# Kernel tuning notes

Hardware: AMD Instinct MI355X
Metric: run time of the kernel (lower is better)

## Reference

```python
import jax, jax.numpy as jnp
import numpy as np

PI = float(np.pi)


def _mat(rows):
    # rows: 4 lists of 4 [..., ] arrays -> [..., 4, 4]
    return jnp.stack([jnp.stack(r, axis=-1) for r in rows], axis=-2)


def _local_frames(q):
    """q: [..., 7] joint angles -> list of 8 local [..., 4, 4] transforms."""
    z = jnp.zeros_like(q[..., 0])
    o = jnp.ones_like(z)

    def cs(a):
        return jnp.cos(a), jnp.sin(a)

    c0, s0 = cs(q[..., 0])
    c1, s1 = cs(q[..., 1])
    c2, s2 = cs(q[..., 2] - 0.5 * PI)
    c3, s3 = cs(q[..., 3])
    c4, s4 = cs(q[..., 4])
    c5, s5 = cs(q[..., 5] + 0.5 * PI)
    c6, s6 = cs(q[..., 6] - 0.5 * PI)

    m0 = _mat([[c0, -s0, z, z], [s0, c0, z, z], [z, z, o, z], [z, z, z, o]])
    m1 = _mat([[c1, -s1, z, z], [z, z, -o, z], [s1, c1, z, z], [z, z, z, o]])
    m2 = _mat([[c2, -s2, z, z], [z, z, o, 0.4 * o], [-s2, -c2, z, z], [z, z, z, o]])
    m3 = _mat([[c3, -s3, z, z], [z, z, -o, z], [s3, c3, z, z], [z, z, z, o]])
    m4 = _mat([[-c4, s4, z, z], [z, z, o, 0.39 * o], [s4, c4, z, z], [z, z, z, o]])
    m5 = _mat([[c5, -s5, z, z], [z, z, -o, z], [s5, c5, z, z], [z, z, z, o]])
    m6 = _mat([[c6, -s6, z, z], [z, z, -o, z], [s6, c6, z, z], [z, z, z, o]])
    m7 = _mat([[-o, z, z, z], [z, z, o, 0.118 * o], [z, o, z, z], [z, z, z, o]])
    return [m0, m1, m2, m3, m4, m5, m6, m7]


def setup_inputs() -> dict:
    key = jax.random.key(0)
    x = jax.random.normal(key, (2000000, 7), dtype=jnp.float32)
    return {"x": x}


def reference(x):
    mats = _local_frames(x)
    frames = [mats[0]]
    f = mats[0]
    for m in mats[1:]:  # fixed chain of 7 tiny 4x4 matmuls over batch
        f = jnp.einsum("...ij,...jk->...ik", f, m)
        frames.append(f)
    return jnp.stack(frames, axis=-3)  # [..., 8, 4, 4]
```

## Files before the change

kernel.cpp:

```cpp
#include <hip/hip_runtime.h>

namespace {

struct V3 { float x, y, z; };

__device__ inline V3 v3(float x, float y, float z) { return {x, y, z}; }
__device__ inline V3 vadd(V3 a, V3 b) { return {a.x + b.x, a.y + b.y, a.z + b.z}; }
__device__ inline V3 vsub(V3 a, V3 b) { return {a.x - b.x, a.y - b.y, a.z - b.z}; }
__device__ inline V3 vmul(float s, V3 a) { return {s * a.x, s * a.y, s * a.z}; }
__device__ inline V3 vneg(V3 a) { return {-a.x, -a.y, -a.z}; }

__device__ inline void stage_frame(float4* p, V3 c0, V3 c1, V3 c2, V3 c3) {
    p[0] = make_float4(c0.x, c1.x, c2.x, c3.x);
    p[1] = make_float4(c0.y, c1.y, c2.y, c3.y);
    p[2] = make_float4(c0.z, c1.z, c2.z, c3.z);
    p[3] = make_float4(0.f, 0.f, 0.f, 1.f);
}

}

#define LSTRIDE 33

__global__ __launch_bounds__(64) void fk_chain_kernel(const float* __restrict__ q,
                                                      float4* __restrict__ out,
                                                      int n)
{
    __shared__ float4 lds[64 * LSTRIDE];

    const int lane = threadIdx.x;
    const long long e0 = (long long)blockIdx.x * 64;
    const long long i = e0 + lane;
    const bool active = i < (long long)n;

    const float* qi = q + (active ? i : (long long)(n - 1)) * 7;
    const float HPI = 1.57079632679489662f;

    float qv[7];
    #pragma unroll
    for (int k = 0; k < 7; ++k) qv[k] = qi[k];

    float c[7], s[7];
    __sincosf(qv[0], &s[0], &c[0]);
    __sincosf(qv[1], &s[1], &c[1]);
    __sincosf(qv[2] - HPI, &s[2], &c[2]);
    __sincosf(qv[3], &s[3], &c[3]);
    __sincosf(qv[4], &s[4], &c[4]);
    __sincosf(qv[5] + HPI, &s[5], &c[5]);
    __sincosf(qv[6] - HPI, &s[6], &c[6]);

    float4* myS = lds + lane * LSTRIDE;

    V3 f0 = v3(c[0], s[0], 0.f);
    V3 f1 = v3(-s[0], c[0], 0.f);
    V3 f2 = v3(0.f, 0.f, 1.f);
    V3 f3 = v3(0.f, 0.f, 0.f);

    #define TYPE_A(cc, ss)                                 \
        {                                                  \
            V3 t0 = vadd(vmul((cc), f0), vmul((ss), f2));  \
            V3 t1 = vsub(vmul((cc), f2), vmul((ss), f0));  \
            V3 t2 = vneg(f1);                              \
            f0 = t0; f1 = t1; f2 = t2;                     \
        }

    stage_frame(myS + 0, f0, f1, f2, f3);

    TYPE_A(c[1], s[1]);
    stage_frame(myS + 4, f0, f1, f2, f3);

    {
        V3 t0 = vsub(vmul(c[2], f0), vmul(s[2], f2));
        V3 t1 = vneg(vadd(vmul(s[2], f0), vmul(c[2], f2)));
        V3 t2 = f1;
        f3 = vadd(vmul(0.4f, f1), f3);
        f0 = t0; f1 = t1; f2 = t2;
    }
    stage_frame(myS + 8, f0, f1, f2, f3);

    TYPE_A(c[3], s[3]);
    stage_frame(myS + 12, f0, f1, f2, f3);

    {
        V3 t0 = vsub(vmul(s[4], f2), vmul(c[4], f0));
        V3 t1 = vadd(vmul(s[4], f0), vmul(c[4], f2));
        V3 t2 = f1;
        f3 = vadd(vmul(0.39f, f1), f3);
        f0 = t0; f1 = t1; f2 = t2;
    }
    stage_frame(myS + 16, f0, f1, f2, f3);

    TYPE_A(c[5], s[5]);
    stage_frame(myS + 20, f0, f1, f2, f3);

    TYPE_A(c[6], s[6]);
    stage_frame(myS + 24, f0, f1, f2, f3);

    {
        V3 t0 = vneg(f0);
        V3 t1 = f2;
        V3 t2 = f1;
        f3 = vadd(vmul(0.118f, f1), f3);
        f0 = t0; f1 = t1; f2 = t2;
    }
    stage_frame(myS + 28, f0, f1, f2, f3);

    #undef TYPE_A

    __syncthreads();

    float4* gb = out + e0 * 32;
    if (e0 + 64 <= (long long)n) {
        #pragma unroll
        for (int j = 0; j < 32; ++j) {
            int flat = j * 64 + lane;
            gb[flat] = lds[(flat >> 5) * LSTRIDE + (flat & 31)];
        }
    } else {
        #pragma unroll
        for (int j = 0; j < 32; ++j) {
            int flat = j * 64 + lane;
            if (e0 + (flat >> 5) < (long long)n)
                gb[flat] = lds[(flat >> 5) * LSTRIDE + (flat & 31)];
        }
    }
}

extern "C" void kernel_launch(void* const* d_in, const int* in_sizes, int n_in,
                              void* d_out, int out_size, void* d_ws, size_t ws_size,
                              hipStream_t stream) {
    const float* x = (const float*)d_in[0];
    float* out = (float*)d_out;
    int n = in_sizes[0] / 7;
    int grid = (n + 63) / 64;
    fk_chain_kernel<<<grid, 64, 0, stream>>>(x, (float4*)out, n);
}
```

Before: 192.8 us.

## Double-buffer LDS across multiple element groups per block and drop constant row staging

Each 64-thread block now handles eight groups of 64 elements, computing the next group into a second LDS buffer while the previous one is written out. Only the three non-constant rows of each 4x4 frame are staged in LDS, and the final [0,0,0,1] row is filled in during the flush. The goal is fewer blocks, less LDS traffic per element, and overlap between compute and global stores. The cost is larger per-block LDS use, fewer resident waves to hide latency, and a barrier per group.

Measured after the change: 214.6 us. 11.3% more time.

```diff
diff --git a/kernel.cpp b/kernel.cpp
--- a/kernel.cpp
+++ b/kernel.cpp
@@ -1,38 +1,27 @@
 #include <hip/hip_runtime.h>
+
+
+#define GROUPS_PER_BLOCK 8
+#define LSTRIDE 25
 
 namespace {
 
 struct V3 { float x, y, z; };
+__device__ __forceinline__ V3 v3(float x, float y, float z) { return {x, y, z}; }
 
-__device__ inline V3 v3(float x, float y, float z) { return {x, y, z}; }
-__device__ inline V3 vadd(V3 a, V3 b) { return {a.x + b.x, a.y + b.y, a.z + b.z}; }
-__device__ inline V3 vsub(V3 a, V3 b) { return {a.x - b.x, a.y - b.y, a.z - b.z}; }
-__device__ inline V3 vmul(float s, V3 a) { return {s * a.x, s * a.y, s * a.z}; }
-__device__ inline V3 vneg(V3 a) { return {-a.x, -a.y, -a.z}; }
-
-__device__ inline void stage_frame(float4* p, V3 c0, V3 c1, V3 c2, V3 c3) {
+__device__ __forceinline__ void stage3(float4* p, V3 c0, V3 c1, V3 c2, V3 c3) {
     p[0] = make_float4(c0.x, c1.x, c2.x, c3.x);
     p[1] = make_float4(c0.y, c1.y, c2.y, c3.y);
     p[2] = make_float4(c0.z, c1.z, c2.z, c3.z);
-    p[3] = make_float4(0.f, 0.f, 0.f, 1.f);
 }
 
-}
-
-#define LSTRIDE 33
-
-__global__ __launch_bounds__(64) void fk_chain_kernel(const float* __restrict__ q,
-                                                      float4* __restrict__ out,
-                                                      int n)
+__device__ __forceinline__ void compute_stage(const float* __restrict__ q,
+                                              float4* __restrict__ buf,
+                                              int lane, long long grp, long long n)
 {
-    __shared__ float4 lds[64 * LSTRIDE];
-
-    const int lane = threadIdx.x;
-    const long long e0 = (long long)blockIdx.x * 64;
-    const long long i = e0 + lane;
-    const bool active = i < (long long)n;
-
-    const float* qi = q + (active ? i : (long long)(n - 1)) * 7;
+    long long i = grp * 64 + lane;
+    if (i >= n) i = n - 1;
+    const float* qi = q + i * 7;
     const float HPI = 1.57079632679489662f;
 
     float qv[7];
@@ -48,81 +37,123 @@
     __sincosf(qv[5] + HPI, &s[5], &c[5]);
     __sincosf(qv[6] - HPI, &s[6], &c[6]);
 
-    float4* myS = lds + lane * LSTRIDE;
+    float4* myS = buf + lane * LSTRIDE;
 
     V3 f0 = v3(c[0], s[0], 0.f);
     V3 f1 = v3(-s[0], c[0], 0.f);
     V3 f2 = v3(0.f, 0.f, 1.f);
     V3 f3 = v3(0.f, 0.f, 0.f);
 
-    #define TYPE_A(cc, ss)                                 \
-        {                                                  \
-            V3 t0 = vadd(vmul((cc), f0), vmul((ss), f2));  \
-            V3 t1 = vsub(vmul((cc), f2), vmul((ss), f0));  \
-            V3 t2 = vneg(f1);                              \
-            f0 = t0; f1 = t1; f2 = t2;                     \
+    #define TYPE_A(cc, ss)                                              \
+        {                                                               \
+            V3 t0 = v3((cc)*f0.x + (ss)*f2.x, (cc)*f0.y + (ss)*f2.y, (cc)*f0.z + (ss)*f2.z); \
+            V3 t1 = v3((cc)*f2.x - (ss)*f0.x, (cc)*f2.y - (ss)*f0.y, (cc)*f2.z - (ss)*f0.z); \
+            V3 t2 = v3(-f1.x, -f1.y, -f1.z);                            \
+            f0 = t0; f1 = t1; f2 = t2;                                  \
         }
 
-    stage_frame(myS + 0, f0, f1, f2, f3);
+    stage3(myS + 0, f0, f1, f2, f3);
 
     TYPE_A(c[1], s[1]);
-    stage_frame(myS + 4, f0, f1, f2, f3);
+    stage3(myS + 3, f0, f1, f2, f3);
 
     {
-        V3 t0 = vsub(vmul(c[2], f0), vmul(s[2], f2));
-        V3 t1 = vneg(vadd(vmul(s[2], f0), vmul(c[2], f2)));
+        V3 t0 = v3(c[2]*f0.x - s[2]*f2.x, c[2]*f0.y - s[2]*f2.y, c[2]*f0.z - s[2]*f2.z);
+        V3 t1 = v3(-(s[2]*f0.x + c[2]*f2.x), -(s[2]*f0.y + c[2]*f2.y), -(s[2]*f0.z + c[2]*f2.z));
         V3 t2 = f1;
-        f3 = vadd(vmul(0.4f, f1), f3);
+        f3 = v3(0.4f*f1.x + f3.x, 0.4f*f1.y + f3.y, 0.4f*f1.z + f3.z);
         f0 = t0; f1 = t1; f2 = t2;
     }
-    stage_frame(myS + 8, f0, f1, f2, f3);
+    stage3(myS + 6, f0, f1, f2, f3);
 
     TYPE_A(c[3], s[3]);
-    stage_frame(myS + 12, f0, f1, f2, f3);
+    stage3(myS + 9, f0, f1, f2, f3);
 
     {
-        V3 t0 = vsub(vmul(s[4], f2), vmul(c[4], f0));
-        V3 t1 = vadd(vmul(s[4], f0), vmul(c[4], f2));
+        V3 t0 = v3(s[4]*f2.x - c[4]*f0.x, s[4]*f2.y - c[4]*f0.y, s[4]*f2.z - c[4]*f0.z);
+        V3 t1 = v3(s[4]*f0.x + c[4]*f2.x, s[4]*f0.y + c[4]*f2.y, s[4]*f0.z + c[4]*f2.z);
         V3 t2 = f1;
-        f3 = vadd(vmul(0.39f, f1), f3);
+        f3 = v3(0.39f*f1.x + f3.x, 0.39f*f1.y + f3.y, 0.39f*f1.z + f3.z);
         f0 = t0; f1 = t1; f2 = t2;
     }
-    stage_frame(myS + 16, f0, f1, f2, f3);
+    stage3(myS + 12, f0, f1, f2, f3);
 
     TYPE_A(c[5], s[5]);
-    stage_frame(myS + 20, f0, f1, f2, f3);
+    stage3(myS + 15, f0, f1, f2, f3);
 
     TYPE_A(c[6], s[6]);
-    stage_frame(myS + 24, f0, f1, f2, f3);
+    stage3(myS + 18, f0, f1, f2, f3);
 
     {
-        V3 t0 = vneg(f0);
+        V3 t0 = v3(-f0.x, -f0.y, -f0.z);
         V3 t1 = f2;
         V3 t2 = f1;
-        f3 = vadd(vmul(0.118f, f1), f3);
+        f3 = v3(0.118f*f1.x + f3.x, 0.118f*f1.y + f3.y, 0.118f*f1.z + f3.z);
         f0 = t0; f1 = t1; f2 = t2;
     }
-    stage_frame(myS + 28, f0, f1, f2, f3);
+    stage3(myS + 21, f0, f1, f2, f3);
 
     #undef TYPE_A
+}
 
-    __syncthreads();
+__device__ __forceinline__ void flush_group(const float4* __restrict__ buf,
+                                            float4* __restrict__ out,
+                                            int lane, long long grp, long long n,
+                                            bool full)
+{
+    const int p  = lane & 31;
+    const int eh = lane >> 5;
+    const int f  = p >> 2;
+    const int r  = p & 3;
+    const int rr = (r == 3) ? 2 : r;
+    const int base_off = eh * LSTRIDE + f * 3 + rr;
+    const bool isr3 = (r == 3);
+    float4* gb = out + grp * 2048;
 
-    float4* gb = out + e0 * 32;
-    if (e0 + 64 <= (long long)n) {
+    if (full) {
         #pragma unroll
         for (int j = 0; j < 32; ++j) {
-            int flat = j * 64 + lane;
-            gb[flat] = lds[(flat >> 5) * LSTRIDE + (flat & 31)];
+            float4 v = buf[j * (2 * LSTRIDE) + base_off];
+            if (isr3) v = make_float4(0.f, 0.f, 0.f, 1.f);
+            gb[j * 64 + lane] = v;
         }
     } else {
         #pragma unroll
         for (int j = 0; j < 32; ++j) {
-            int flat = j * 64 + lane;
-            if (e0 + (flat >> 5) < (long long)n)
-                gb[flat] = lds[(flat >> 5) * LSTRIDE + (flat & 31)];
+            float4 v = buf[j * (2 * LSTRIDE) + base_off];
+            if (isr3) v = make_float4(0.f, 0.f, 0.f, 1.f);
+            long long e = (long long)((j * 64 + lane) >> 5);
+            if (grp * 64 + e < n) gb[j * 64 + lane] = v;
         }
     }
+}
+
+}
+
+__global__ __launch_bounds__(64) void fk_chain_kernel(const float* __restrict__ q,
+                                                      float4* __restrict__ out,
+                                                      int n, int ngroups)
+{
+    __shared__ float4 lds[2][64 * LSTRIDE];
+
+    const int lane = threadIdx.x;
+    const long long g0 = (long long)blockIdx.x * GROUPS_PER_BLOCK;
+    if (g0 >= ngroups) return;
+    const int ng = (ngroups - g0 < GROUPS_PER_BLOCK) ? (int)(ngroups - g0)
+                                                     : GROUPS_PER_BLOCK;
+
+    compute_stage(q, lds[0], lane, g0, n);
+    int cur = 0;
+    for (int t = 1; t < ng; ++t) {
+        __syncthreads();
+        compute_stage(q, lds[cur ^ 1], lane, g0 + t, n);
+        bool full = ((g0 + t - 1) * 64 + 64 <= (long long)n);
+        flush_group(lds[cur], out, lane, g0 + t - 1, n, full);
+        cur ^= 1;
+    }
+    __syncthreads();
+    bool full = ((g0 + ng - 1) * 64 + 64 <= (long long)n);
+    flush_group(lds[cur], out, lane, g0 + ng - 1, n, full);
 }
 
 extern "C" void kernel_launch(void* const* d_in, const int* in_sizes, int n_in,
@@ -131,6 +162,7 @@
     const float* x = (const float*)d_in[0];
     float* out = (float*)d_out;
     int n = in_sizes[0] / 7;
-    int grid = (n + 63) / 64;
-    fk_chain_kernel<<<grid, 64, 0, stream>>>(x, (float4*)out, n);
+    int ngroups = (n + 63) >> 6;
+    int grid = (ngroups + GROUPS_PER_BLOCK - 1) / GROUPS_PER_BLOCK;
+    fk_chain_kernel<<<grid, 64, 0, stream>>>(x, (float4*)out, n, ngroups);
 }
```
